# Optimization experiments

Hardware: AMD Instinct MI355X
Metric: run time of the kernel (lower is better)

Reference implementation:

```python
import jax
jax.config.update("jax_enable_x64", True)  # hash needs int64 like torch .long()
import jax.numpy as jnp
import numpy as np

N = 4_194_304
TABLE = 4096
EMB = 16
HID = 64


def setup_inputs() -> dict:
    key = jax.random.key(0)
    ks = jax.random.split(key, 9)
    pos = jax.random.normal(ks[0], (N, 3), jnp.float32)
    normal = jax.random.normal(ks[1], (N, 3), jnp.float32)
    emb = jax.random.normal(ks[2], (TABLE, EMB), jnp.float32) * 0.02
    W1 = jax.random.normal(ks[3], (EMB + 3, HID), jnp.float32) * (1.0 / np.sqrt(EMB + 3))
    b1 = jnp.zeros((HID,), jnp.float32)
    W2 = jax.random.normal(ks[4], (HID, HID), jnp.float32) * (1.0 / np.sqrt(HID))
    b2 = jnp.zeros((HID,), jnp.float32)
    W3 = jax.random.normal(ks[5], (HID, 3), jnp.float32) * (1.0 / np.sqrt(HID))
    b3 = jnp.zeros((3,), jnp.float32)
    return {"pos": pos, "normal": normal, "emb": emb,
            "W1": W1, "b1": b1, "W2": W2, "b2": b2, "W3": W3, "b3": b3}


def _hash_index(pos):
    # torch (pos*10).long() truncates toward zero; astype(int64) matches.
    scaled = (pos * 10.0).astype(jnp.int64)  # [N,3]
    h = (scaled[:, 0] * 73856093) ^ (scaled[:, 1] * 19349663) ^ (scaled[:, 2] * 83492791)
    # jnp.mod and torch % both return result with sign of divisor (nonneg here)
    return jnp.mod(h, TABLE)


def reference(pos, normal, emb, W1, b1, W2, b2, W3, b3):
    idx = _hash_index(pos)            # [N] int64 in [0, 4096)
    feat = emb[idx]                   # [N,16] gather
    x = jnp.concatenate([feat, normal], axis=-1)  # [N,19]
    h = jax.nn.relu(x @ W1 + b1)      # [N,64]
    h = jax.nn.relu(h @ W2 + b2)      # [N,64]
    return jax.nn.sigmoid(h @ W3 + b3)  # [N,3]
```

## Files before the change

### kernel.cpp

```cpp
#include <hip/hip_runtime.h>
#include <hip/hip_bf16.h>
#include <math.h>


typedef __attribute__((ext_vector_type(4)))  float        float4v;
typedef __attribute__((ext_vector_type(4)))  unsigned int uint4v;

#define WSF_OFF   0
#define WSB_OFF   (14 * 64 * 16)
#define EMB_OFF   (WSB_OFF + 5 * 64 * 16)

static __device__ __forceinline__ unsigned fbits(float x) {
    union { float f; unsigned u; } c; c.f = x; return c.u;
}
static __device__ __forceinline__ unsigned pack2_rh(float a, float b) {
    return __builtin_amdgcn_perm(fbits(b) + 0x8000u, fbits(a) + 0x8000u, 0x07060302u);
}
static __device__ __forceinline__ unsigned pack2_rne(float a, float b) {
    __hip_bfloat16 ha = __float2bfloat16(a), hb = __float2bfloat16(b);
    unsigned short ua = *reinterpret_cast<unsigned short*>(&ha);
    unsigned short ub = *reinterpret_cast<unsigned short*>(&hb);
    return (unsigned)ua | ((unsigned)ub << 16);
}
static __device__ __forceinline__ uint4v mk_frag_u(const float* v) {
    uint4v u;
    u.x = pack2_rne(v[0], v[1]); u.y = pack2_rne(v[2], v[3]);
    u.z = pack2_rne(v[4], v[5]); u.w = pack2_rne(v[6], v[7]);
    return u;
}

__global__ void nc_prep(const float* __restrict__ W1, const float* __restrict__ b1,
                        const float* __restrict__ W2, const float* __restrict__ b2,
                        const float* __restrict__ W3, const float* __restrict__ b3,
                        const float* __restrict__ emb, char* __restrict__ ws)
{
    uint4v*   wsf   = (uint4v*)(ws + WSF_OFF);
    float4v*  wsb   = (float4v*)(ws + WSB_OFF);
    unsigned* embbf = (unsigned*)(ws + EMB_OFF);

    const int gtid = blockIdx.x * blockDim.x + threadIdx.x;
    if (gtid < 32768)
        embbf[gtid] = pack2_rne(emb[2 * gtid], emb[2 * gtid + 1]);

    if (blockIdx.x != 0 || threadIdx.x >= 64) return;
    const int lane = threadIdx.x;
    const int m    = lane & 15;
    const int quad = lane >> 4;
    const int qs = m >> 2, rs = m & 3;

    for (int nt = 0; nt < 4; ++nt) {
        const int n = 32 * (nt >> 1) + 8 * qs + 4 * (nt & 1) + rs;
        float v[8];
        for (int j = 0; j < 8; ++j) {
            const int k = quad * 8 + j;
            v[j] = (k < 19) ? W1[k * 64 + n] : (k == 19 ? b1[n] : 0.0f);
        }
        wsf[nt * 64 + lane] = mk_frag_u(v);
    }
    for (int kt = 0; kt < 2; ++kt)
        for (int nt = 0; nt < 4; ++nt) {
            const int n = 32 * (nt >> 1) + 8 * qs + 4 * (nt & 1) + rs;
            float v[8];
            for (int j = 0; j < 8; ++j)
                v[j] = W2[(kt * 32 + quad * 8 + j) * 64 + n];
            wsf[(4 + kt * 4 + nt) * 64 + lane] = mk_frag_u(v);
        }
    for (int kt = 0; kt < 2; ++kt) {
        float v[8];
        for (int j = 0; j < 8; ++j)
            v[j] = (m < 3) ? W3[(kt * 32 + quad * 8 + j) * 3 + m] : 0.0f;
        wsf[(12 + kt) * 64 + lane] = mk_frag_u(v);
    }
    for (int nt = 0; nt < 4; ++nt) {
        const int base = 32 * (nt >> 1) + 8 * quad + 4 * (nt & 1);
        float4v v; v.x = b2[base]; v.y = b2[base+1]; v.z = b2[base+2]; v.w = b2[base+3];
        wsb[nt * 64 + lane] = v;
    }
    float4v v3;
    v3.x = (quad == 0) ? b3[0] : 0.f;
    v3.y = (quad == 0) ? b3[1] : 0.f;
    v3.z = (quad == 0) ? b3[2] : 0.f;
    v3.w = 0.f;
    wsb[4 * 64 + lane] = v3;
}

__global__ __launch_bounds__(256, 3) void nc_mfma6(
    const float* __restrict__ pos, const float* __restrict__ nrm,
    const char* __restrict__ ws, float* __restrict__ out, int npts)
{
    const uint4v*  wsf   = (const uint4v*)(ws + WSF_OFF);
    const float4v* wsb   = (const float4v*)(ws + WSB_OFF);
    const char*    embbf = ws + EMB_OFF;

    const int lane = threadIdx.x & 63;
    const int m    = lane & 15;
    const int quad = lane >> 4;

    uint4v w1p[4], w2p[2][4], w3p[2];
    float4v b2p[4], b3p;
    float4v zerof = (float4v){0.f, 0.f, 0.f, 0.f};
    #pragma unroll
    for (int nt = 0; nt < 4; ++nt) w1p[nt] = wsf[nt * 64 + lane];
    #pragma unroll
    for (int kt = 0; kt < 2; ++kt)
        #pragma unroll
        for (int nt = 0; nt < 4; ++nt)
            w2p[kt][nt] = wsf[(4 + kt * 4 + nt) * 64 + lane];
    #pragma unroll
    for (int kt = 0; kt < 2; ++kt) w3p[kt] = wsf[(12 + kt) * 64 + lane];
    #pragma unroll
    for (int nt = 0; nt < 4; ++nt) b2p[nt] = wsb[nt * 64 + lane];
    b3p = wsb[4 * 64 + lane];

    asm volatile("" : "+a"(w1p[0]), "+a"(w1p[1]), "+a"(w1p[2]), "+a"(w1p[3]));
    asm volatile("" : "+a"(w2p[0][0]), "+a"(w2p[0][1]), "+a"(w2p[0][2]), "+a"(w2p[0][3]));
    asm volatile("" : "+a"(w2p[1][0]), "+a"(w2p[1][1]), "+a"(w2p[1][2]), "+a"(w2p[1][3]));
    asm volatile("" : "+a"(w3p[0]), "+a"(w3p[1]));
    asm volatile("" : "+v"(b2p[0]), "+v"(b2p[1]), "+v"(b2p[2]), "+v"(b2p[3]));
    asm volatile("" : "+v"(b3p), "+v"(zerof));

    const int tilesTotal = npts >> 4;
    const int waveId     = blockIdx.x * 4 + (threadIdx.x >> 6);
    const int numWaves   = gridDim.x * 4;

    int t = waveId;
    float p0 = 0.f, p1 = 0.f, p2 = 0.f, n0 = 0.f, n1 = 0.f, n2 = 0.f;
    if (t < tilesTotal) {
        const int pt = t * 16 + m;
        p0 = pos[3 * pt + 0]; p1 = pos[3 * pt + 1]; p2 = pos[3 * pt + 2];
        n0 = nrm[3 * pt + 0]; n1 = nrm[3 * pt + 1]; n2 = nrm[3 * pt + 2];
    }

    for (; t < tilesTotal; t += numWaves) {
        const int pt = t * 16 + m;

        const int sx = (int)(p0 * 10.0f);
        const int sy = (int)(p1 * 10.0f);
        const int sz = (int)(p2 * 10.0f);
        const unsigned h = ((unsigned)sx * 73856093u)
                         ^ ((unsigned)sy * 19349663u)
                         ^ ((unsigned)sz * 83492791u);
        const unsigned idx = h & 4095u;

        const uint4v ex = *(const uint4v*)(embbf + idx * 32 + ((quad & 1) << 4));
        const unsigned np0 = pack2_rh(n0, n1);
        const unsigned np1 = pack2_rh(n2, 1.0f);
        const bool lt2 = (quad < 2), is2 = (quad == 2);
        uint4v xu;
        xu.x = lt2 ? ex.x : (is2 ? np0 : 0u);
        xu.y = lt2 ? ex.y : (is2 ? np1 : 0u);
        xu.z = lt2 ? ex.z : 0u;
        xu.w = lt2 ? ex.w : 0u;

        {
            const int tn = t + numWaves;
            const int ptn = ((tn < tilesTotal) ? tn : t) * 16 + m;
            p0 = pos[3 * ptn + 0]; p1 = pos[3 * ptn + 1]; p2 = pos[3 * ptn + 2];
            n0 = nrm[3 * ptn + 0]; n1 = nrm[3 * ptn + 1]; n2 = nrm[3 * ptn + 2];
        }

        float4v h1_0, h1_1, h1_2, h1_3;
        asm("s_nop 1\n\t"
            "v_mfma_f32_16x16x32_bf16 %0, %4, %8, %9\n\t"
            "v_mfma_f32_16x16x32_bf16 %1, %5, %8, %9\n\t"
            "v_mfma_f32_16x16x32_bf16 %2, %6, %8, %9\n\t"
            "v_mfma_f32_16x16x32_bf16 %3, %7, %8, %9\n\t"
            "s_nop 7\n\ts_nop 7"
            : "=&v"(h1_0), "=&v"(h1_1), "=&v"(h1_2), "=&v"(h1_3)
            : "a"(w1p[0]), "a"(w1p[1]), "a"(w1p[2]), "a"(w1p[3]),
              "v"(xu), "v"(zerof));

        unsigned q10 = pack2_rh(fmaxf(h1_0.x, 0.f), fmaxf(h1_0.y, 0.f));
        unsigned q11 = pack2_rh(fmaxf(h1_0.z, 0.f), fmaxf(h1_0.w, 0.f));
        unsigned q12 = pack2_rh(fmaxf(h1_1.x, 0.f), fmaxf(h1_1.y, 0.f));
        unsigned q13 = pack2_rh(fmaxf(h1_1.z, 0.f), fmaxf(h1_1.w, 0.f));
        unsigned q14 = pack2_rh(fmaxf(h1_2.x, 0.f), fmaxf(h1_2.y, 0.f));
        unsigned q15 = pack2_rh(fmaxf(h1_2.z, 0.f), fmaxf(h1_2.w, 0.f));
        unsigned q16 = pack2_rh(fmaxf(h1_3.x, 0.f), fmaxf(h1_3.y, 0.f));
        unsigned q17 = pack2_rh(fmaxf(h1_3.z, 0.f), fmaxf(h1_3.w, 0.f));
        uint4v B10; B10.x = q10; B10.y = q11; B10.z = q12; B10.w = q13;
        uint4v B11; B11.x = q14; B11.y = q15; B11.z = q16; B11.w = q17;

        float4v h2_0, h2_1, h2_2, h2_3;
        asm("s_nop 1\n\t"
            "v_mfma_f32_16x16x32_bf16 %0, %4, %12, %14\n\t"
            "v_mfma_f32_16x16x32_bf16 %1, %5, %12, %15\n\t"
            "v_mfma_f32_16x16x32_bf16 %2, %6, %12, %16\n\t"
            "v_mfma_f32_16x16x32_bf16 %3, %7, %12, %17\n\t"
            "v_mfma_f32_16x16x32_bf16 %0, %8, %13, %0\n\t"
            "v_mfma_f32_16x16x32_bf16 %1, %9, %13, %1\n\t"
            "v_mfma_f32_16x16x32_bf16 %2, %10, %13, %2\n\t"
            "v_mfma_f32_16x16x32_bf16 %3, %11, %13, %3\n\t"
            "s_nop 7\n\ts_nop 7"
            : "=&v"(h2_0), "=&v"(h2_1), "=&v"(h2_2), "=&v"(h2_3)
            : "a"(w2p[0][0]), "a"(w2p[0][1]), "a"(w2p[0][2]), "a"(w2p[0][3]),
              "a"(w2p[1][0]), "a"(w2p[1][1]), "a"(w2p[1][2]), "a"(w2p[1][3]),
              "v"(B10), "v"(B11),
              "v"(b2p[0]), "v"(b2p[1]), "v"(b2p[2]), "v"(b2p[3]));

        unsigned q20 = pack2_rh(fmaxf(h2_0.x, 0.f), fmaxf(h2_0.y, 0.f));
        unsigned q21 = pack2_rh(fmaxf(h2_0.z, 0.f), fmaxf(h2_0.w, 0.f));
        unsigned q22 = pack2_rh(fmaxf(h2_1.x, 0.f), fmaxf(h2_1.y, 0.f));
        unsigned q23 = pack2_rh(fmaxf(h2_1.z, 0.f), fmaxf(h2_1.w, 0.f));
        unsigned q24 = pack2_rh(fmaxf(h2_2.x, 0.f), fmaxf(h2_2.y, 0.f));
        unsigned q25 = pack2_rh(fmaxf(h2_2.z, 0.f), fmaxf(h2_2.w, 0.f));
        unsigned q26 = pack2_rh(fmaxf(h2_3.x, 0.f), fmaxf(h2_3.y, 0.f));
        unsigned q27 = pack2_rh(fmaxf(h2_3.z, 0.f), fmaxf(h2_3.w, 0.f));
        uint4v B20; B20.x = q20; B20.y = q21; B20.z = q22; B20.w = q23;
        uint4v B21; B21.x = q24; B21.y = q25; B21.z = q26; B21.w = q27;

        float4v lg;
        asm("s_nop 1\n\t"
            "v_mfma_f32_16x16x32_bf16 %0, %1, %3, %5\n\t"
            "v_mfma_f32_16x16x32_bf16 %0, %2, %4, %0\n\t"
            "s_nop 7\n\ts_nop 7"
            : "=&v"(lg)
            : "a"(w3p[0]), "a"(w3p[1]), "v"(B20), "v"(B21), "v"(b3p));

        if (quad == 0) {
            const float s0 = 1.0f / (1.0f + __expf(-lg.x));
            const float s1 = 1.0f / (1.0f + __expf(-lg.y));
            const float s2 = 1.0f / (1.0f + __expf(-lg.z));
            float* o = out + 3 * pt;
            o[0] = s0; o[1] = s1; o[2] = s2;
        }
    }
}

extern "C" void kernel_launch(void* const* d_in, const int* in_sizes, int n_in,
                              void* d_out, int out_size, void* d_ws, size_t ws_size,
                              hipStream_t stream) {
    const float* pos = (const float*)d_in[0];
    const float* nrm = (const float*)d_in[1];
    const float* emb = (const float*)d_in[2];
    const float* W1  = (const float*)d_in[3];
    const float* b1  = (const float*)d_in[4];
    const float* W2  = (const float*)d_in[5];
    const float* b2  = (const float*)d_in[6];
    const float* W3  = (const float*)d_in[7];
    const float* b3  = (const float*)d_in[8];
    float* out = (float*)d_out;

    const int npts = in_sizes[0] / 3;

    nc_prep<<<128, 256, 0, stream>>>(W1, b1, W2, b2, W3, b3, emb, (char*)d_ws);
    nc_mfma6<<<768, 256, 0, stream>>>(pos, nrm, (const char*)d_ws, out, npts);
}
```

Before: 267.9 us.

## Process 64-point groups per wave with lane-parallel hashing and bpermute redistribution

Each wave now loads and hashes 64 points at once, one per lane, and uses ds_bpermute to hand embedding offsets and packed normals to the 16-row MFMA layout over four inner sub-tiles. Before, only 16 of the 64 lanes did useful load and hash work per tile. The manual round-half bf16 packing is replaced by the hardware v_cvt_pk_bf16_f32 instruction. Occupancy is raised to 4 blocks per CU with a 1024-block grid. The change adds LDS-crossbar permute traffic and register pressure, and the new launch bounds could cause register spills.

```diff
diff --git a/kernel.cpp b/kernel.cpp
--- a/kernel.cpp
+++ b/kernel.cpp
@@ -10,12 +10,6 @@
 #define WSB_OFF   (14 * 64 * 16)
 #define EMB_OFF   (WSB_OFF + 5 * 64 * 16)
 
-static __device__ __forceinline__ unsigned fbits(float x) {
-    union { float f; unsigned u; } c; c.f = x; return c.u;
-}
-static __device__ __forceinline__ unsigned pack2_rh(float a, float b) {
-    return __builtin_amdgcn_perm(fbits(b) + 0x8000u, fbits(a) + 0x8000u, 0x07060302u);
-}
 static __device__ __forceinline__ unsigned pack2_rne(float a, float b) {
     __hip_bfloat16 ha = __float2bfloat16(a), hb = __float2bfloat16(b);
     unsigned short ua = *reinterpret_cast<unsigned short*>(&ha);
@@ -27,6 +21,11 @@
     u.x = pack2_rne(v[0], v[1]); u.y = pack2_rne(v[2], v[3]);
     u.z = pack2_rne(v[4], v[5]); u.w = pack2_rne(v[6], v[7]);
     return u;
+}
+static __device__ __forceinline__ unsigned cvtpk(float a, float b) {
+    unsigned r;
+    asm("v_cvt_pk_bf16_f32 %0, %1, %2" : "=v"(r) : "v"(a), "v"(b));
+    return r;
 }
 
 __global__ void nc_prep(const float* __restrict__ W1, const float* __restrict__ b1,
@@ -84,7 +83,7 @@
     wsb[4 * 64 + lane] = v3;
 }
 
-__global__ __launch_bounds__(256, 3) void nc_mfma6(
+__global__ __launch_bounds__(256, 4) void nc_mfma7(
     const float* __restrict__ pos, const float* __restrict__ nrm,
     const char* __restrict__ ws, float* __restrict__ out, int npts)
 {
@@ -119,20 +118,24 @@
     asm volatile("" : "+v"(b2p[0]), "+v"(b2p[1]), "+v"(b2p[2]), "+v"(b2p[3]));
     asm volatile("" : "+v"(b3p), "+v"(zerof));
 
-    const int tilesTotal = npts >> 4;
-    const int waveId     = blockIdx.x * 4 + (threadIdx.x >> 6);
-    const int numWaves   = gridDim.x * 4;
-
-    int t = waveId;
+    const int groupsTotal = npts >> 6;
+    const int waveId      = blockIdx.x * 4 + (threadIdx.x >> 6);
+    const int numWaves    = gridDim.x * 4;
+
+    const int  a0   = m << 2;
+    const bool is2  = (quad == 2);
+    const int  esel = (quad & 1) << 4;
+
+    int g = waveId;
     float p0 = 0.f, p1 = 0.f, p2 = 0.f, n0 = 0.f, n1 = 0.f, n2 = 0.f;
-    if (t < tilesTotal) {
-        const int pt = t * 16 + m;
+    if (g < groupsTotal) {
+        const int pt = g * 64 + lane;
         p0 = pos[3 * pt + 0]; p1 = pos[3 * pt + 1]; p2 = pos[3 * pt + 2];
         n0 = nrm[3 * pt + 0]; n1 = nrm[3 * pt + 1]; n2 = nrm[3 * pt + 2];
     }
 
-    for (; t < tilesTotal; t += numWaves) {
-        const int pt = t * 16 + m;
+    for (; g < groupsTotal; g += numWaves) {
+        const int base3 = g * 192;
 
         const int sx = (int)(p0 * 10.0f);
         const int sy = (int)(p1 * 10.0f);
@@ -140,89 +143,96 @@
         const unsigned h = ((unsigned)sx * 73856093u)
                          ^ ((unsigned)sy * 19349663u)
                          ^ ((unsigned)sz * 83492791u);
-        const unsigned idx = h & 4095u;
-
-        const uint4v ex = *(const uint4v*)(embbf + idx * 32 + ((quad & 1) << 4));
-        const unsigned np0 = pack2_rh(n0, n1);
-        const unsigned np1 = pack2_rh(n2, 1.0f);
-        const bool lt2 = (quad < 2), is2 = (quad == 2);
-        uint4v xu;
-        xu.x = lt2 ? ex.x : (is2 ? np0 : 0u);
-        xu.y = lt2 ? ex.y : (is2 ? np1 : 0u);
-        xu.z = lt2 ? ex.z : 0u;
-        xu.w = lt2 ? ex.w : 0u;
+        const int idxb = (int)((h & 4095u) << 5);
+
+        const unsigned np0 = cvtpk(n0, n1);
+        const unsigned np1 = cvtpk(n2, 1.0f);
 
         {
-            const int tn = t + numWaves;
-            const int ptn = ((tn < tilesTotal) ? tn : t) * 16 + m;
+            const int tn  = g + numWaves;
+            const int ptn = ((tn < groupsTotal) ? tn : g) * 64 + lane;
             p0 = pos[3 * ptn + 0]; p1 = pos[3 * ptn + 1]; p2 = pos[3 * ptn + 2];
             n0 = nrm[3 * ptn + 0]; n1 = nrm[3 * ptn + 1]; n2 = nrm[3 * ptn + 2];
         }
 
-        float4v h1_0, h1_1, h1_2, h1_3;
-        asm("s_nop 1\n\t"
-            "v_mfma_f32_16x16x32_bf16 %0, %4, %8, %9\n\t"
-            "v_mfma_f32_16x16x32_bf16 %1, %5, %8, %9\n\t"
-            "v_mfma_f32_16x16x32_bf16 %2, %6, %8, %9\n\t"
-            "v_mfma_f32_16x16x32_bf16 %3, %7, %8, %9\n\t"
-            "s_nop 7\n\ts_nop 7"
-            : "=&v"(h1_0), "=&v"(h1_1), "=&v"(h1_2), "=&v"(h1_3)
-            : "a"(w1p[0]), "a"(w1p[1]), "a"(w1p[2]), "a"(w1p[3]),
-              "v"(xu), "v"(zerof));
-
-        unsigned q10 = pack2_rh(fmaxf(h1_0.x, 0.f), fmaxf(h1_0.y, 0.f));
-        unsigned q11 = pack2_rh(fmaxf(h1_0.z, 0.f), fmaxf(h1_0.w, 0.f));
-        unsigned q12 = pack2_rh(fmaxf(h1_1.x, 0.f), fmaxf(h1_1.y, 0.f));
-        unsigned q13 = pack2_rh(fmaxf(h1_1.z, 0.f), fmaxf(h1_1.w, 0.f));
-        unsigned q14 = pack2_rh(fmaxf(h1_2.x, 0.f), fmaxf(h1_2.y, 0.f));
-        unsigned q15 = pack2_rh(fmaxf(h1_2.z, 0.f), fmaxf(h1_2.w, 0.f));
-        unsigned q16 = pack2_rh(fmaxf(h1_3.x, 0.f), fmaxf(h1_3.y, 0.f));
-        unsigned q17 = pack2_rh(fmaxf(h1_3.z, 0.f), fmaxf(h1_3.w, 0.f));
-        uint4v B10; B10.x = q10; B10.y = q11; B10.z = q12; B10.w = q13;
-        uint4v B11; B11.x = q14; B11.y = q15; B11.z = q16; B11.w = q17;
-
-        float4v h2_0, h2_1, h2_2, h2_3;
-        asm("s_nop 1\n\t"
-            "v_mfma_f32_16x16x32_bf16 %0, %4, %12, %14\n\t"
-            "v_mfma_f32_16x16x32_bf16 %1, %5, %12, %15\n\t"
-            "v_mfma_f32_16x16x32_bf16 %2, %6, %12, %16\n\t"
-            "v_mfma_f32_16x16x32_bf16 %3, %7, %12, %17\n\t"
-            "v_mfma_f32_16x16x32_bf16 %0, %8, %13, %0\n\t"
-            "v_mfma_f32_16x16x32_bf16 %1, %9, %13, %1\n\t"
-            "v_mfma_f32_16x16x32_bf16 %2, %10, %13, %2\n\t"
-            "v_mfma_f32_16x16x32_bf16 %3, %11, %13, %3\n\t"
-            "s_nop 7\n\ts_nop 7"
-            : "=&v"(h2_0), "=&v"(h2_1), "=&v"(h2_2), "=&v"(h2_3)
-            : "a"(w2p[0][0]), "a"(w2p[0][1]), "a"(w2p[0][2]), "a"(w2p[0][3]),
-              "a"(w2p[1][0]), "a"(w2p[1][1]), "a"(w2p[1][2]), "a"(w2p[1][3]),
-              "v"(B10), "v"(B11),
-              "v"(b2p[0]), "v"(b2p[1]), "v"(b2p[2]), "v"(b2p[3]));
-
-        unsigned q20 = pack2_rh(fmaxf(h2_0.x, 0.f), fmaxf(h2_0.y, 0.f));
-        unsigned q21 = pack2_rh(fmaxf(h2_0.z, 0.f), fmaxf(h2_0.w, 0.f));
-        unsigned q22 = pack2_rh(fmaxf(h2_1.x, 0.f), fmaxf(h2_1.y, 0.f));
-        unsigned q23 = pack2_rh(fmaxf(h2_1.z, 0.f), fmaxf(h2_1.w, 0.f));
-        unsigned q24 = pack2_rh(fmaxf(h2_2.x, 0.f), fmaxf(h2_2.y, 0.f));
-        unsigned q25 = pack2_rh(fmaxf(h2_2.z, 0.f), fmaxf(h2_2.w, 0.f));
-        unsigned q26 = pack2_rh(fmaxf(h2_3.x, 0.f), fmaxf(h2_3.y, 0.f));
-        unsigned q27 = pack2_rh(fmaxf(h2_3.z, 0.f), fmaxf(h2_3.w, 0.f));
-        uint4v B20; B20.x = q20; B20.y = q21; B20.z = q22; B20.w = q23;
-        uint4v B21; B21.x = q24; B21.y = q25; B21.z = q26; B21.w = q27;
-
-        float4v lg;
-        asm("s_nop 1\n\t"
-            "v_mfma_f32_16x16x32_bf16 %0, %1, %3, %5\n\t"
-            "v_mfma_f32_16x16x32_bf16 %0, %2, %4, %0\n\t"
-            "s_nop 7\n\ts_nop 7"
-            : "=&v"(lg)
-            : "a"(w3p[0]), "a"(w3p[1]), "v"(B20), "v"(B21), "v"(b3p));
-
-        if (quad == 0) {
-            const float s0 = 1.0f / (1.0f + __expf(-lg.x));
-            const float s1 = 1.0f / (1.0f + __expf(-lg.y));
-            const float s2 = 1.0f / (1.0f + __expf(-lg.z));
-            float* o = out + 3 * pt;
-            o[0] = s0; o[1] = s1; o[2] = s2;
+        #pragma unroll 1
+        for (int j = 0; j < 4; ++j) {
+            const int bj = a0 + (j << 6);
+
+            const int      eoff = __builtin_amdgcn_ds_bpermute(bj, idxb);
+            const unsigned p0j  = (unsigned)__builtin_amdgcn_ds_bpermute(bj, (int)np0);
+            const unsigned p1j  = (unsigned)__builtin_amdgcn_ds_bpermute(bj, (int)np1);
+
+            const uint4v ex = *(const uint4v*)(embbf + eoff + esel);
+            uint4v xu;
+            xu.x = is2 ? p0j : ex.x;
+            xu.y = is2 ? p1j : ex.y;
+            xu.z = ex.z;
+            xu.w = ex.w;
+
+            float4v h1_0, h1_1, h1_2, h1_3;
+            asm("s_nop 1\n\t"
+                "v_mfma_f32_16x16x32_bf16 %0, %4, %8, %9\n\t"
+                "v_mfma_f32_16x16x32_bf16 %1, %5, %8, %9\n\t"
+                "v_mfma_f32_16x16x32_bf16 %2, %6, %8, %9\n\t"
+                "v_mfma_f32_16x16x32_bf16 %3, %7, %8, %9\n\t"
+                "s_nop 7\n\ts_nop 7"
+                : "=&v"(h1_0), "=&v"(h1_1), "=&v"(h1_2), "=&v"(h1_3)
+                : "a"(w1p[0]), "a"(w1p[1]), "a"(w1p[2]), "a"(w1p[3]),
+                  "v"(xu), "v"(zerof));
+
+            uint4v B10, B11;
+            B10.x = cvtpk(fmaxf(h1_0.x, 0.f), fmaxf(h1_0.y, 0.f));
+            B10.y = cvtpk(fmaxf(h1_0.z, 0.f), fmaxf(h1_0.w, 0.f));
+            B10.z = cvtpk(fmaxf(h1_1.x, 0.f), fmaxf(h1_1.y, 0.f));
+            B10.w = cvtpk(fmaxf(h1_1.z, 0.f), fmaxf(h1_1.w, 0.f));
+            B11.x = cvtpk(fmaxf(h1_2.x, 0.f), fmaxf(h1_2.y, 0.f));
+            B11.y = cvtpk(fmaxf(h1_2.z, 0.f), fmaxf(h1_2.w, 0.f));
+            B11.z = cvtpk(fmaxf(h1_3.x, 0.f), fmaxf(h1_3.y, 0.f));
+            B11.w = cvtpk(fmaxf(h1_3.z, 0.f), fmaxf(h1_3.w, 0.f));
+
+            float4v h2_0, h2_1, h2_2, h2_3;
+            asm("s_nop 1\n\t"
+                "v_mfma_f32_16x16x32_bf16 %0, %4, %12, %14\n\t"
+                "v_mfma_f32_16x16x32_bf16 %1, %5, %12, %15\n\t"
+                "v_mfma_f32_16x16x32_bf16 %2, %6, %12, %16\n\t"
+                "v_mfma_f32_16x16x32_bf16 %3, %7, %12, %17\n\t"
+                "v_mfma_f32_16x16x32_bf16 %0, %8, %13, %0\n\t"
+                "v_mfma_f32_16x16x32_bf16 %1, %9, %13, %1\n\t"
+                "v_mfma_f32_16x16x32_bf16 %2, %10, %13, %2\n\t"
+                "v_mfma_f32_16x16x32_bf16 %3, %11, %13, %3\n\t"
+                "s_nop 7\n\ts_nop 7"
+                : "=&v"(h2_0), "=&v"(h2_1), "=&v"(h2_2), "=&v"(h2_3)
+                : "a"(w2p[0][0]), "a"(w2p[0][1]), "a"(w2p[0][2]), "a"(w2p[0][3]),
+                  "a"(w2p[1][0]), "a"(w2p[1][1]), "a"(w2p[1][2]), "a"(w2p[1][3]),
+                  "v"(B10), "v"(B11),
+                  "v"(b2p[0]), "v"(b2p[1]), "v"(b2p[2]), "v"(b2p[3]));
+
+            uint4v B20, B21;
+            B20.x = cvtpk(fmaxf(h2_0.x, 0.f), fmaxf(h2_0.y, 0.f));
+            B20.y = cvtpk(fmaxf(h2_0.z, 0.f), fmaxf(h2_0.w, 0.f));
+            B20.z = cvtpk(fmaxf(h2_1.x, 0.f), fmaxf(h2_1.y, 0.f));
+            B20.w = cvtpk(fmaxf(h2_1.z, 0.f), fmaxf(h2_1.w, 0.f));
+            B21.x = cvtpk(fmaxf(h2_2.x, 0.f), fmaxf(h2_2.y, 0.f));
+            B21.y = cvtpk(fmaxf(h2_2.z, 0.f), fmaxf(h2_2.w, 0.f));
+            B21.z = cvtpk(fmaxf(h2_3.x, 0.f), fmaxf(h2_3.y, 0.f));
+            B21.w = cvtpk(fmaxf(h2_3.z, 0.f), fmaxf(h2_3.w, 0.f));
+
+            float4v lg;
+            asm("s_nop 1\n\t"
+                "v_mfma_f32_16x16x32_bf16 %0, %1, %3, %5\n\t"
+                "v_mfma_f32_16x16x32_bf16 %0, %2, %4, %0\n\t"
+                "s_nop 7\n\ts_nop 7"
+                : "=&v"(lg)
+                : "a"(w3p[0]), "a"(w3p[1]), "v"(B20), "v"(B21), "v"(b3p));
+
+            if (quad == 0) {
+                const float s0 = 1.0f / (1.0f + __expf(-lg.x));
+                const float s1 = 1.0f / (1.0f + __expf(-lg.y));
+                const float s2 = 1.0f / (1.0f + __expf(-lg.z));
+                float* o = out + base3 + j * 48 + 3 * m;
+                o[0] = s0; o[1] = s1; o[2] = s2;
+            }
         }
     }
 }
@@ -244,5 +254,5 @@
     const int npts = in_sizes[0] / 3;
 
     nc_prep<<<128, 256, 0, stream>>>(W1, b1, W2, b2, W3, b3, emb, (char*)d_ws);
-    nc_mfma6<<<768, 256, 0, stream>>>(pos, nrm, (const char*)d_ws, out, npts);
-}
+    nc_mfma7<<<1024, 256, 0, stream>>>(pos, nrm, (const char*)d_ws, out, npts);
+}
```

Result: faster. 234.5 us (-12.5%).
